# Kernel optimization log

Measured on AMD Instinct MI355X. Metric: run time of the kernel, lower is better.

## Reference

```python
import jax, jax.numpy as jnp
import numpy as np

N_NODES = 100000
N_EDGES = 1600000
D_IN = 256
HID = 128
OUT = 16
EPS = 1e-5


def _layer_norm(h, g, b):
    mu = jnp.mean(h, axis=-1, keepdims=True)
    var = jnp.mean((h - mu) ** 2, axis=-1, keepdims=True)
    return (h - mu) * jax.lax.rsqrt(var + EPS) * g + b


def _sage_conv(h, src, dst, Wn, bn, Wr):
    # mean-aggregate neighbor (source) features onto destination nodes
    msg = h[src]                                                # [E, F]
    s = jax.ops.segment_sum(msg, dst, num_segments=N_NODES)     # [N, F]
    cnt = jax.ops.segment_sum(jnp.ones((src.shape[0],), h.dtype), dst, num_segments=N_NODES)
    mean = s / jnp.maximum(cnt, 1.0)[:, None]
    return mean @ Wn + bn + h @ Wr                              # lin_l(agg) + lin_r(x)


def setup_inputs() -> dict:
    key = jax.random.key(0)
    ks = jax.random.split(key, 16)
    def lin(k, fi, fo):
        return jax.random.normal(k, (fi, fo), jnp.float32) / np.sqrt(fi)
    x = jax.random.normal(ks[0], (N_NODES, D_IN), jnp.float32)
    edge_index = jax.random.randint(ks[1], (2, N_EDGES), 0, N_NODES, dtype=jnp.int64)
    return {
        "x": x, "edge_index": edge_index,
        "W_nl0": lin(ks[2], D_IN, HID), "b_nl0": jnp.zeros((HID,), jnp.float32),
        "W_r0": lin(ks[3], D_IN, HID),
        "W_nl1": lin(ks[4], HID, HID), "b_nl1": jnp.zeros((HID,), jnp.float32),
        "W_r1": lin(ks[5], HID, HID),
        "g0": jnp.ones((HID,), jnp.float32), "be0": jnp.zeros((HID,), jnp.float32),
        "g1": jnp.ones((HID,), jnp.float32), "be1": jnp.zeros((HID,), jnp.float32),
        "W_jk": lin(ks[6], 2 * HID, HID), "b_jk": jnp.zeros((HID,), jnp.float32),
        "W_h1": lin(ks[7], HID, HID // 4), "b_h1": jnp.zeros((HID // 4,), jnp.float32),
        "W_h2": lin(ks[8], HID // 4, OUT), "b_h2": jnp.zeros((OUT,), jnp.float32),
    }


def reference(x, edge_index, W_nl0, b_nl0, W_r0, W_nl1, b_nl1, W_r1,
              g0, be0, g1, be1, W_jk, b_jk, W_h1, b_h1, W_h2, b_h2):
    src, dst = edge_index[0], edge_index[1]
    # layer 0: conv -> LayerNorm -> ReLU (dropout = identity in eval)
    h0 = jax.nn.relu(_layer_norm(_sage_conv(x, src, dst, W_nl0, b_nl0, W_r0), g0, be0))
    # layer 1
    h1 = jax.nn.relu(_layer_norm(_sage_conv(h0, src, dst, W_nl1, b_nl1, W_r1), g1, be1))
    # jumping-knowledge concat + projection to hidden_dim
    feats = jnp.concatenate([h0, h1], axis=-1) @ W_jk + b_jk
    # MLP head
    out = jax.nn.relu(feats @ W_h1 + b_h1) @ W_h2 + b_h2
    return out
```

## Files before the change

### kernel.cpp

```cpp
#include <hip/hip_runtime.h>
#include <hip/hip_bf16.h>

typedef __attribute__((ext_vector_type(8))) short bf16x8;
typedef __attribute__((ext_vector_type(4))) float f32x4;

static __device__ __forceinline__ float bf2f(__hip_bfloat16 v) { return __bfloat162float(v); }

static __device__ __forceinline__ float bs2f(short s) {
    unsigned u = ((unsigned)(unsigned short)s) << 16;
    float f; __builtin_memcpy(&f, &u, 4); return f;
}
static __device__ __forceinline__ short f2bs(float v) {
    __hip_bfloat16 b = __float2bfloat16(v);
    short s; __builtin_memcpy(&s, &b, 2); return s;
}
static __device__ __forceinline__ float loadf(const void* p, int i, bool f32) {
    if (f32) return ((const float*)p)[i];
    return bf2f(((const __hip_bfloat16*)p)[i]);
}

__global__ __launch_bounds__(256) void detect_kernel(const unsigned* __restrict__ ew,
        const unsigned short* __restrict__ xw, int* __restrict__ flags) {
    __shared__ int s_odd, s_f32;
    int t = threadIdx.x;
    if (t == 0) { s_odd = 0; s_f32 = 0; }
    __syncthreads();
    unsigned acc = 0;
    for (int i = t; i < 2048; i += 256) acc |= ew[2 * i + 1];
    if (acc) atomicOr(&s_odd, 1);
    int f32ev = 0;
    for (int i = t; i < 4096; i += 256) {
        unsigned e = (xw[i] >> 7) & 0xFF;
        if (e >= 0xC0) f32ev = 1;
    }
    if (f32ev) atomicOr(&s_f32, 1);
    __syncthreads();
    if (t == 0) { flags[0] = s_odd ? 0 : 1; flags[1] = s_f32; }
}


static __device__ __forceinline__ int dec_src(const unsigned* ew, int E, bool i64, int e) {
    return i64 ? (int)ew[2 * (size_t)e] : (int)ew[e];
}
static __device__ __forceinline__ int dec_dst(const unsigned* ew, int E, bool i64, int e) {
    return i64 ? (int)ew[2 * (size_t)E + 2 * (size_t)e] : (int)ew[(size_t)E + e];
}

__global__ __launch_bounds__(256) void coarse_count(const unsigned* __restrict__ ew, int E,
        const int* __restrict__ flags, int* __restrict__ ccnt) {
    __shared__ int h[512];
    int tid = threadIdx.x;
    for (int i = tid; i < 512; i += 256) h[i] = 0;
    __syncthreads();
    bool i64 = flags[0] != 0;
    int base = blockIdx.x * 8192;
    int lim = min(base + 8192, E);
    for (int e = base + tid; e < lim; e += 256)
        atomicAdd(&h[dec_dst(ew, E, i64, e) >> 8], 1);
    __syncthreads();
    for (int i = tid; i < 512; i += 256) if (h[i]) atomicAdd(&ccnt[i], h[i]);
}

__global__ __launch_bounds__(256) void coarse_scan(const int* __restrict__ ccnt,
        int* __restrict__ cbase, int* __restrict__ ccur, int NBINS) {
    __shared__ int part[256];
    int t = threadIdx.x;
    int v0 = (2 * t     < NBINS) ? ccnt[2 * t]     : 0;
    int v1 = (2 * t + 1 < NBINS) ? ccnt[2 * t + 1] : 0;
    int sum = v0 + v1;
    part[t] = sum;
    __syncthreads();
    for (int off = 1; off < 256; off <<= 1) {
        int u = (t >= off) ? part[t - off] : 0;
        __syncthreads();
        part[t] += u;
        __syncthreads();
    }
    int run = part[t] - sum;
    if (2 * t < NBINS)     { cbase[2 * t] = run;     ccur[2 * t] = run; }
    run += v0;
    if (2 * t + 1 < NBINS) { cbase[2 * t + 1] = run; ccur[2 * t + 1] = run; }
    if (t == 255) cbase[NBINS] = part[255];
}

__global__ __launch_bounds__(256) void coarse_scatter(const unsigned* __restrict__ ew, int E,
        const int* __restrict__ flags, int* __restrict__ ccur,
        uint2* __restrict__ pairs, int NBINS) {
    __shared__ int hist[512];
    __shared__ int hscan[513];
    __shared__ int fbase[512];
    __shared__ int part[256];
    __shared__ uint2 stage[2048];
    int tid = threadIdx.x;
    bool i64 = flags[0] != 0;
    int base = blockIdx.x * 2048;
    int cnt = min(2048, E - base);
    for (int i = tid; i < 512; i += 256) hist[i] = 0;
    __syncthreads();
    int myb[8], myo[8], mys[8], myd[8];
    #pragma unroll
    for (int j = 0; j < 8; ++j) {
        int e = base + j * 256 + tid;
        myb[j] = -1;
        if (e < E) {
            mys[j] = dec_src(ew, E, i64, e);
            int d = dec_dst(ew, E, i64, e);
            myd[j] = d & 255;
            myb[j] = d >> 8;
            myo[j] = atomicAdd(&hist[myb[j]], 1);
        }
    }
    __syncthreads();
    {
        int v0 = hist[2 * tid], v1 = hist[2 * tid + 1];
        int sum = v0 + v1;
        part[tid] = sum;
        __syncthreads();
        for (int off = 1; off < 256; off <<= 1) {
            int u = (tid >= off) ? part[tid - off] : 0;
            __syncthreads();
            part[tid] += u;
            __syncthreads();
        }
        int run = part[tid] - sum;
        hscan[2 * tid] = run;
        hscan[2 * tid + 1] = run + v0;
        if (tid == 255) hscan[512] = part[255];
    }
    __syncthreads();
    #pragma unroll
    for (int j = 0; j < 8; ++j)
        if (myb[j] >= 0) {
            uint2 p; p.x = (unsigned)mys[j]; p.y = (unsigned)myd[j];
            stage[hscan[myb[j]] + myo[j]] = p;
        }
    for (int i = tid; i < NBINS; i += 256) {
        int c = hist[i];
        if (c) fbase[i] = atomicAdd(&ccur[i], c);
    }
    __syncthreads();
    for (int i = tid; i < cnt; i += 256) {
        int lo = 0, hi = NBINS;
        while (hi - lo > 1) {
            int mid = (lo + hi) >> 1;
            if (hscan[mid] <= i) lo = mid; else hi = mid;
        }
        pairs[(size_t)fbase[lo] + (i - hscan[lo])] = stage[i];
    }
}

__global__ __launch_bounds__(256) void bin_degree(const uint2* __restrict__ pairs,
        const int* __restrict__ cbase, int* __restrict__ deg, int N) {
    __shared__ int dl[256];
    int tid = threadIdx.x, b = blockIdx.x;
    dl[tid] = 0;
    __syncthreads();
    int s = cbase[b], e = cbase[b + 1];
    for (int i = s + tid; i < e; i += 256) atomicAdd(&dl[pairs[i].y], 1);
    __syncthreads();
    int node = (b << 8) + tid;
    if (node < N) deg[node] = dl[tid];
}

__global__ __launch_bounds__(256) void bin_scatter(const uint2* __restrict__ pairs,
        const int* __restrict__ cbase, const int* __restrict__ rowptr,
        int* __restrict__ ebuf, int N) {
    __shared__ int cur[256];
    int tid = threadIdx.x, b = blockIdx.x;
    int node = (b << 8) + tid;
    cur[tid] = (node < N) ? rowptr[node] : 0;
    __syncthreads();
    int s = cbase[b], e = cbase[b + 1];
    for (int i = s + tid; i < e; i += 256) {
        uint2 p = pairs[i];
        int pos = atomicAdd(&cur[p.y], 1);
        ebuf[pos] = (int)p.x;
    }
}

__global__ __launch_bounds__(256) void scan_phaseA(const int* __restrict__ deg,
        int* __restrict__ blocksum, int N) {
    __shared__ int red[256];
    int i0 = blockIdx.x * 512 + threadIdx.x * 2;
    int s = 0;
    if (i0 < N)     s += deg[i0];
    if (i0 + 1 < N) s += deg[i0 + 1];
    red[threadIdx.x] = s;
    __syncthreads();
    for (int off = 128; off; off >>= 1) {
        if (threadIdx.x < off) red[threadIdx.x] += red[threadIdx.x + off];
        __syncthreads();
    }
    if (threadIdx.x == 0) blocksum[blockIdx.x] = red[0];
}

__global__ __launch_bounds__(256) void scan_phaseB(int* __restrict__ blocksum, int NB,
        int* __restrict__ rowptr, int N) {
    __shared__ int part[256];
    int t = threadIdx.x;
    int v[4]; int sum = 0;
    #pragma unroll
    for (int j = 0; j < 4; ++j) {
        int i = 4 * t + j;
        v[j] = (i < NB) ? blocksum[i] : 0;
        sum += v[j];
    }
    part[t] = sum;
    __syncthreads();
    for (int off = 1; off < 256; off <<= 1) {
        int u = (t >= off) ? part[t - off] : 0;
        __syncthreads();
        part[t] += u;
        __syncthreads();
    }
    int run = part[t] - sum;
    #pragma unroll
    for (int j = 0; j < 4; ++j) {
        int i = 4 * t + j;
        if (i < NB) blocksum[i] = run;
        run += v[j];
    }
    if (t == 255) rowptr[N] = part[255];
}

__global__ __launch_bounds__(256) void scan_phaseC(const int* __restrict__ deg,
        const int* __restrict__ blockoff, int* __restrict__ rowptr, int N) {
    __shared__ int part[256];
    int t = threadIdx.x;
    int i0 = blockIdx.x * 512 + 2 * t;
    int d0 = (i0 < N)     ? deg[i0]     : 0;
    int d1 = (i0 + 1 < N) ? deg[i0 + 1] : 0;
    int sum = d0 + d1;
    part[t] = sum;
    __syncthreads();
    for (int off = 1; off < 256; off <<= 1) {
        int u = (t >= off) ? part[t - off] : 0;
        __syncthreads();
        part[t] += u;
        __syncthreads();
    }
    int run = blockoff[blockIdx.x] + part[t] - sum;
    if (i0 < N)     rowptr[i0] = run;
    run += d0;
    if (i0 + 1 < N) rowptr[i0 + 1] = run;
}

__global__ void transpose_kernel(const void* __restrict__ W,
        __hip_bfloat16* __restrict__ Wt, int rows, int cols, int ldt,
        const int* __restrict__ flags) {
    int idx = blockIdx.x * blockDim.x + threadIdx.x;
    if (idx < rows * cols) {
        int fi = idx / cols, fo = idx % cols;
        Wt[fo * ldt + fi] = __float2bfloat16(loadf(W, idx, flags[1] != 0));
    }
}

template<int KSTEPS>
__global__ __launch_bounds__(256) void gemm_v6(
        const void* __restrict__ X0, const void* __restrict__ X1, int K0, int xflag,
        const __hip_bfloat16* __restrict__ Wt, const void* __restrict__ bias,
        void* __restrict__ outp, int ldo, int out_f32, int M, int Ncols,
        const int* __restrict__ flags) {
    constexpr int K = KSTEPS * 32;
    constexpr int CH = K / 8;
    constexpr int SITERS = (64 * CH) / 256;
    __shared__ short Wf[4 * KSTEPS * 64 * 8];
    bool pf = flags[1] != 0;
    bool xf32 = (xflag != 0) && pf;
    int tid = threadIdx.x;
    int wave = tid >> 6, lane = tid & 63;
    int quad = lane >> 4, r = lane & 15;
    int nodeA = blockIdx.x * 128 + wave * 32 + r;
    int nodeB = nodeA + 16;
    int nA = min(nodeA, M - 1);
    int nB = min(nodeB, M - 1);

    bf16x8 xfA[KSTEPS], xfB[KSTEPS];
    if (xf32) {
        #pragma unroll
        for (int ks = 0; ks < KSTEPS; ++ks) {
            int k = ks * 32 + quad * 8;
            const float* pA = (k < K0)
                ? ((const float*)X0 + (size_t)nA * K0 + k)
                : ((const float*)X1 + (size_t)nA * (K - K0) + (k - K0));
            const float* pB = (k < K0)
                ? ((const float*)X0 + (size_t)nB * K0 + k)
                : ((const float*)X1 + (size_t)nB * (K - K0) + (k - K0));
            float4 a0 = *(const float4*)pA;
            float4 a1 = *(const float4*)(pA + 4);
            float4 b0 = *(const float4*)pB;
            float4 b1 = *(const float4*)(pB + 4);
            bf16x8 ta, tb;
            ta[0] = f2bs(a0.x); ta[1] = f2bs(a0.y); ta[2] = f2bs(a0.z); ta[3] = f2bs(a0.w);
            ta[4] = f2bs(a1.x); ta[5] = f2bs(a1.y); ta[6] = f2bs(a1.z); ta[7] = f2bs(a1.w);
            tb[0] = f2bs(b0.x); tb[1] = f2bs(b0.y); tb[2] = f2bs(b0.z); tb[3] = f2bs(b0.w);
            tb[4] = f2bs(b1.x); tb[5] = f2bs(b1.y); tb[6] = f2bs(b1.z); tb[7] = f2bs(b1.w);
            xfA[ks] = ta;
            xfB[ks] = tb;
        }
    } else {
        #pragma unroll
        for (int ks = 0; ks < KSTEPS; ++ks) {
            int k = ks * 32 + quad * 8;
            const __hip_bfloat16* pA = (k < K0)
                ? ((const __hip_bfloat16*)X0 + (size_t)nA * K0 + k)
                : ((const __hip_bfloat16*)X1 + (size_t)nA * (K - K0) + (k - K0));
            const __hip_bfloat16* pB = (k < K0)
                ? ((const __hip_bfloat16*)X0 + (size_t)nB * K0 + k)
                : ((const __hip_bfloat16*)X1 + (size_t)nB * (K - K0) + (k - K0));
            xfA[ks] = *(const bf16x8*)pA;
            xfB[ks] = *(const bf16x8*)pB;
        }
    }

    int nphases = Ncols >> 6;
    for (int p = 0; p < nphases; ++p) {
        if (p) __syncthreads();
        #pragma unroll
        for (int i = 0; i < SITERS; ++i) {
            int idx = i * 256 + tid;
            int row_l = idx / CH, c = idx % CH;
            uint4 v = *(const uint4*)((const short*)Wt + (size_t)(p * 64 + row_l) * K + c * 8);
            int ftl = row_l >> 4, rr = row_l & 15;
            int ks = c >> 2, q = c & 3;
            int chunk = ((q * 16 + rr) ^ ks);
            *(uint4*)(Wf + (size_t)(((ftl * KSTEPS + ks) * 64) + chunk) * 8) = v;
        }
        __syncthreads();
        #pragma unroll
        for (int ftl = 0; ftl < 4; ++ftl) {
            f32x4 accA = {0.f, 0.f, 0.f, 0.f};
            f32x4 accB = {0.f, 0.f, 0.f, 0.f};
            #pragma unroll
            for (int ks = 0; ks < KSTEPS; ++ks) {
                bf16x8 wf = *(const bf16x8*)(Wf + (size_t)((ftl * KSTEPS + ks) * 64 + (lane ^ ks)) * 8);
                accA = __builtin_amdgcn_mfma_f32_16x16x32_bf16(wf, xfA[ks], accA, 0, 0, 0);
                accB = __builtin_amdgcn_mfma_f32_16x16x32_bf16(wf, xfB[ks], accB, 0, 0, 0);
            }
            int fo = p * 64 + ftl * 16 + quad * 4;
            float b0 = 0.f, b1 = 0.f, b2 = 0.f, b3 = 0.f;
            if (bias) {
                b0 = loadf(bias, fo + 0, pf); b1 = loadf(bias, fo + 1, pf);
                b2 = loadf(bias, fo + 2, pf); b3 = loadf(bias, fo + 3, pf);
            }
            if (out_f32) {
                if (nodeA < M) {
                    float4 res;
                    res.x = accA[0] + b0; res.y = accA[1] + b1;
                    res.z = accA[2] + b2; res.w = accA[3] + b3;
                    *(float4*)((float*)outp + (size_t)nodeA * ldo + fo) = res;
                }
                if (nodeB < M) {
                    float4 res;
                    res.x = accB[0] + b0; res.y = accB[1] + b1;
                    res.z = accB[2] + b2; res.w = accB[3] + b3;
                    *(float4*)((float*)outp + (size_t)nodeB * ldo + fo) = res;
                }
            } else {
                if (nodeA < M) {
                    short4 res;
                    res.x = f2bs(accA[0] + b0); res.y = f2bs(accA[1] + b1);
                    res.z = f2bs(accA[2] + b2); res.w = f2bs(accA[3] + b3);
                    *(short4*)((short*)outp + (size_t)nodeA * ldo + fo) = res;
                }
                if (nodeB < M) {
                    short4 res;
                    res.x = f2bs(accB[0] + b0); res.y = f2bs(accB[1] + b1);
                    res.z = f2bs(accB[2] + b2); res.w = f2bs(accB[3] + b3);
                    *(short4*)((short*)outp + (size_t)nodeB * ldo + fo) = res;
                }
            }
        }
    }
}

__global__ __launch_bounds__(256) void agg_ln_relu(
        const __hip_bfloat16* __restrict__ yz, const int* __restrict__ rowptr,
        const int* __restrict__ ebuf,
        const void* __restrict__ bn, const void* __restrict__ g,
        const void* __restrict__ be, __hip_bfloat16* __restrict__ hout, int N,
        const int* __restrict__ flags) {
    int node = (blockIdx.x * blockDim.x + threadIdx.x) >> 6;
    if (node >= N) return;
    node = __builtin_amdgcn_readfirstlane(node);
    bool pf = flags[1] != 0;
    int lane = threadIdx.x & 63;
    int f = lane * 2;
    const short* yzs = (const short*)yz;
    int start = rowptr[node], end = rowptr[node + 1];
    float a0 = 0.f, a1 = 0.f;
    int i = start;
    for (; i + 8 <= end; i += 8) {
        int n0 = ebuf[i + 0], n1 = ebuf[i + 1], n2 = ebuf[i + 2], n3 = ebuf[i + 3];
        int n4 = ebuf[i + 4], n5 = ebuf[i + 5], n6 = ebuf[i + 6], n7 = ebuf[i + 7];
        short2 t0 = *(const short2*)(yzs + (size_t)n0 * 256 + f);
        short2 t1 = *(const short2*)(yzs + (size_t)n1 * 256 + f);
        short2 t2 = *(const short2*)(yzs + (size_t)n2 * 256 + f);
        short2 t3 = *(const short2*)(yzs + (size_t)n3 * 256 + f);
        short2 t4 = *(const short2*)(yzs + (size_t)n4 * 256 + f);
        short2 t5 = *(const short2*)(yzs + (size_t)n5 * 256 + f);
        short2 t6 = *(const short2*)(yzs + (size_t)n6 * 256 + f);
        short2 t7 = *(const short2*)(yzs + (size_t)n7 * 256 + f);
        a0 += bs2f(t0.x) + bs2f(t1.x) + bs2f(t2.x) + bs2f(t3.x)
            + bs2f(t4.x) + bs2f(t5.x) + bs2f(t6.x) + bs2f(t7.x);
        a1 += bs2f(t0.y) + bs2f(t1.y) + bs2f(t2.y) + bs2f(t3.y)
            + bs2f(t4.y) + bs2f(t5.y) + bs2f(t6.y) + bs2f(t7.y);
    }
    for (; i + 2 <= end; i += 2) {
        int n0 = ebuf[i + 0], n1 = ebuf[i + 1];
        short2 t0 = *(const short2*)(yzs + (size_t)n0 * 256 + f);
        short2 t1 = *(const short2*)(yzs + (size_t)n1 * 256 + f);
        a0 += bs2f(t0.x) + bs2f(t1.x);
        a1 += bs2f(t0.y) + bs2f(t1.y);
    }
    if (i < end) {
        int n0 = ebuf[i];
        short2 t0 = *(const short2*)(yzs + (size_t)n0 * 256 + f);
        a0 += bs2f(t0.x);
        a1 += bs2f(t0.y);
    }
    float inv = 1.f / fmaxf((float)(end - start), 1.f);
    short2 zt = *(const short2*)(yzs + (size_t)node * 256 + 128 + f);
    float v0 = a0 * inv + loadf(bn, f, pf)     + bs2f(zt.x);
    float v1 = a1 * inv + loadf(bn, f + 1, pf) + bs2f(zt.y);
    float s = v0 + v1;
    #pragma unroll
    for (int off = 32; off > 0; off >>= 1) s += __shfl_xor(s, off, 64);
    float mu = s * (1.f / 128.f);
    float d0 = v0 - mu, d1 = v1 - mu;
    float q = d0 * d0 + d1 * d1;
    #pragma unroll
    for (int off = 32; off > 0; off >>= 1) q += __shfl_xor(q, off, 64);
    float rstd = rsqrtf(q * (1.f / 128.f) + 1e-5f);
    float o0 = fmaxf(d0 * rstd * loadf(g, f, pf)     + loadf(be, f, pf),     0.f);
    float o1 = fmaxf(d1 * rstd * loadf(g, f + 1, pf) + loadf(be, f + 1, pf), 0.f);
    short* hp = (short*)hout + (size_t)node * 128 + f;
    hp[0] = f2bs(o0);
    hp[1] = f2bs(o1);
}

__global__ __launch_bounds__(256) void head_kernel(
        const float* __restrict__ feats, const void* __restrict__ Wh1,
        const void* __restrict__ bh1, const void* __restrict__ Wh2,
        const void* __restrict__ bh2, void* __restrict__ outp, int N,
        const int* __restrict__ flags) {
    __shared__ float sfe[8 * 128];
    __shared__ float shid[8 * 32];
    bool pf = flags[1] != 0;
    int nb = blockIdx.x * 8;
    int tid = threadIdx.x;
    {
        int i = tid * 4;
        int gnode = nb + (i >> 7);
        float4 v = make_float4(0.f, 0.f, 0.f, 0.f);
        if (gnode < N) v = *(const float4*)(feats + (size_t)gnode * 128 + (i & 127));
        *(float4*)(sfe + i) = v;
    }
    __syncthreads();
    {
        int nloc = tid >> 5, col = tid & 31;
        float acc = loadf(bh1, col, pf);
        const float* fr = sfe + nloc * 128;
        #pragma unroll 8
        for (int k = 0; k < 128; ++k) acc += fr[k] * loadf(Wh1, k * 32 + col, pf);
        shid[nloc * 32 + col] = fmaxf(acc, 0.f);
    }
    __syncthreads();
    if (tid < 128) {
        int nloc = tid >> 4, col = tid & 15;
        int gnode = nb + nloc;
        if (gnode < N) {
            float acc = loadf(bh2, col, pf);
            const float* hr = shid + nloc * 32;
            #pragma unroll
            for (int k = 0; k < 32; ++k) acc += hr[k] * loadf(Wh2, k * 16 + col, pf);
            if (pf) ((float*)outp)[(size_t)gnode * 16 + col] = acc;
            else    ((__hip_bfloat16*)outp)[(size_t)gnode * 16 + col] = __float2bfloat16(acc);
        }
    }
}

extern "C" void kernel_launch(void* const* d_in, const int* in_sizes, int n_in,
                              void* d_out, int out_size, void* d_ws, size_t ws_size,
                              hipStream_t stream) {
    const void* x    = d_in[0];
    const unsigned* ei = (const unsigned*)d_in[1];
    const void* Wnl0 = d_in[2];
    const void* bnl0 = d_in[3];
    const void* Wr0  = d_in[4];
    const void* Wnl1 = d_in[5];
    const void* bnl1 = d_in[6];
    const void* Wr1  = d_in[7];
    const void* g0   = d_in[8];
    const void* be0  = d_in[9];
    const void* g1   = d_in[10];
    const void* be1  = d_in[11];
    const void* Wjk  = d_in[12];
    const void* bjk  = d_in[13];
    const void* Wh1  = d_in[14];
    const void* bh1  = d_in[15];
    const void* Wh2  = d_in[16];
    const void* bh2  = d_in[17];

    const int N = in_sizes[0] / 256;
    const int E = in_sizes[1] / 2;
    const int NBINS = (N + 255) >> 8;

    char* ws = (char*)d_ws;
    size_t off = 0;
    auto alloc = [&](size_t bytes) -> void* {
        void* p = ws + off;
        off = (off + bytes + 255) & ~(size_t)255;
        return p;
    };
    int* flags  = (int*)alloc(256);
    int* rowptr = (int*)alloc((size_t)(N + 1) * 4);
    int* deg    = (int*)alloc((size_t)N * 4);
    int* ebuf   = (int*)alloc((size_t)E * 4);
    int* blocksum = (int*)alloc(1024 * 4);
    int* ccnt   = (int*)alloc(512 * 4);
    int* cbase  = (int*)alloc(513 * 4);
    int* ccur   = (int*)alloc(512 * 4);
    uint2* pairs = (uint2*)alloc((size_t)E * 8);
    __hip_bfloat16* Wt0  = (__hip_bfloat16*)alloc(256 * 256 * 2);
    __hip_bfloat16* Wt1  = (__hip_bfloat16*)alloc(256 * 128 * 2);
    __hip_bfloat16* Wtjk = (__hip_bfloat16*)alloc(128 * 256 * 2);
    __hip_bfloat16* yz = (__hip_bfloat16*)alloc((size_t)N * 256 * 2);
    __hip_bfloat16* h0 = (__hip_bfloat16*)alloc((size_t)N * 128 * 2);
    __hip_bfloat16* h1 = (__hip_bfloat16*)alloc((size_t)N * 128 * 2);
    float* feats = (float*)yz;

    detect_kernel<<<1, 256, 0, stream>>>(ei, (const unsigned short*)x, flags);

    (void)hipMemsetAsync(ccnt, 0, 512 * 4, stream);
    coarse_count<<<(E + 8191) / 8192, 256, 0, stream>>>(ei, E, flags, ccnt);
    coarse_scan<<<1, 256, 0, stream>>>(ccnt, cbase, ccur, NBINS);
    coarse_scatter<<<(E + 2047) / 2048, 256, 0, stream>>>(ei, E, flags, ccur, pairs, NBINS);
    bin_degree<<<NBINS, 256, 0, stream>>>(pairs, cbase, deg, N);
    int NB = (N + 511) / 512;
    scan_phaseA<<<NB, 256, 0, stream>>>(deg, blocksum, N);
    scan_phaseB<<<1, 256, 0, stream>>>(blocksum, NB, rowptr, N);
    scan_phaseC<<<NB, 256, 0, stream>>>(deg, blocksum, rowptr, N);
    bin_scatter<<<NBINS, 256, 0, stream>>>(pairs, cbase, rowptr, ebuf, N);

    transpose_kernel<<<(256 * 128 + 255) / 256, 256, 0, stream>>>(Wnl0, Wt0, 256, 128, 256, flags);
    transpose_kernel<<<(256 * 128 + 255) / 256, 256, 0, stream>>>(Wr0,  Wt0 + 128 * 256, 256, 128, 256, flags);
    transpose_kernel<<<(128 * 128 + 255) / 256, 256, 0, stream>>>(Wnl1, Wt1, 128, 128, 128, flags);
    transpose_kernel<<<(128 * 128 + 255) / 256, 256, 0, stream>>>(Wr1,  Wt1 + 128 * 128, 128, 128, 128, flags);
    transpose_kernel<<<(256 * 128 + 255) / 256, 256, 0, stream>>>(Wjk,  Wtjk, 256, 128, 256, flags);

    int gblocks = (N + 127) / 128;
    int ablocks = (int)(((size_t)N * 64 + 255) / 256);

    gemm_v6<8><<<gblocks, 256, 0, stream>>>(x, x, 256, 1, Wt0, nullptr, yz, 256, 0, N, 256, flags);
    agg_ln_relu<<<ablocks, 256, 0, stream>>>(yz, rowptr, ebuf, bnl0, g0, be0, h0, N, flags);

    gemm_v6<4><<<gblocks, 256, 0, stream>>>(h0, h0, 128, 0, Wt1, nullptr, yz, 256, 0, N, 256, flags);
    agg_ln_relu<<<ablocks, 256, 0, stream>>>(yz, rowptr, ebuf, bnl1, g1, be1, h1, N, flags);

    gemm_v6<8><<<gblocks, 256, 0, stream>>>(h0, h1, 128, 0, Wtjk, bjk, feats, 128, 1, N, 128, flags);

    head_kernel<<<(N + 7) / 8, 256, 0, stream>>>(feats, Wh1, bh1, Wh2, bh2, d_out, N, flags);
}
```

Baseline: 574.1 us.

## Run MLP head first layer on MFMA with transposed bf16 weights

Replaces the scalar head kernel, which did 8 nodes per block with per-thread scalar dot products, with a version that handles 128 nodes per block. It converts feats to bf16 fragments and uses 16x16x32 bf16 MFMA for the 128->32 layer, staging a transposed Wh1 in swizzled LDS. The second 32->16 layer stays scalar, with vectorized output stores. This adds a small transpose launch and rounds the first-layer inputs to bf16, which may change accuracy slightly.

```diff
diff --git a/kernel.cpp b/kernel.cpp
--- a/kernel.cpp
+++ b/kernel.cpp
@@ -37,7 +37,6 @@
     __syncthreads();
     if (t == 0) { flags[0] = s_odd ? 0 : 1; flags[1] = s_f32; }
 }
-
 
 static __device__ __forceinline__ int dec_src(const unsigned* ew, int E, bool i64, int e) {
     return i64 ? (int)ew[2 * (size_t)e] : (int)ew[e];
@@ -439,43 +438,105 @@
     hp[1] = f2bs(o1);
 }
 
-__global__ __launch_bounds__(256) void head_kernel(
-        const float* __restrict__ feats, const void* __restrict__ Wh1,
+__global__ __launch_bounds__(256) void head_v2(
+        const float* __restrict__ feats, const __hip_bfloat16* __restrict__ Wth1,
         const void* __restrict__ bh1, const void* __restrict__ Wh2,
         const void* __restrict__ bh2, void* __restrict__ outp, int N,
         const int* __restrict__ flags) {
-    __shared__ float sfe[8 * 128];
-    __shared__ float shid[8 * 32];
+    constexpr int KSTEPS = 4;
+    constexpr int CH = 16;
+    constexpr int HS = 34;
+    __shared__ short Wf[2 * KSTEPS * 64 * 8];
+    __shared__ float hid[128 * HS];
     bool pf = flags[1] != 0;
-    int nb = blockIdx.x * 8;
     int tid = threadIdx.x;
-    {
-        int i = tid * 4;
-        int gnode = nb + (i >> 7);
-        float4 v = make_float4(0.f, 0.f, 0.f, 0.f);
-        if (gnode < N) v = *(const float4*)(feats + (size_t)gnode * 128 + (i & 127));
-        *(float4*)(sfe + i) = v;
-    }
-    __syncthreads();
-    {
-        int nloc = tid >> 5, col = tid & 31;
-        float acc = loadf(bh1, col, pf);
-        const float* fr = sfe + nloc * 128;
-        #pragma unroll 8
-        for (int k = 0; k < 128; ++k) acc += fr[k] * loadf(Wh1, k * 32 + col, pf);
-        shid[nloc * 32 + col] = fmaxf(acc, 0.f);
-    }
-    __syncthreads();
-    if (tid < 128) {
-        int nloc = tid >> 4, col = tid & 15;
-        int gnode = nb + nloc;
-        if (gnode < N) {
-            float acc = loadf(bh2, col, pf);
-            const float* hr = shid + nloc * 32;
-            #pragma unroll
-            for (int k = 0; k < 32; ++k) acc += hr[k] * loadf(Wh2, k * 16 + col, pf);
-            if (pf) ((float*)outp)[(size_t)gnode * 16 + col] = acc;
-            else    ((__hip_bfloat16*)outp)[(size_t)gnode * 16 + col] = __float2bfloat16(acc);
+    int wave = tid >> 6, lane = tid & 63;
+    int quad = lane >> 4, r = lane & 15;
+    int nodeA = blockIdx.x * 128 + wave * 32 + r;
+    int nodeB = nodeA + 16;
+    int nA = min(nodeA, N - 1);
+    int nB = min(nodeB, N - 1);
+
+    bf16x8 xfA[KSTEPS], xfB[KSTEPS];
+    #pragma unroll
+    for (int ks = 0; ks < KSTEPS; ++ks) {
+        int k = ks * 32 + quad * 8;
+        const float* pA = feats + (size_t)nA * 128 + k;
+        const float* pB = feats + (size_t)nB * 128 + k;
+        float4 a0 = *(const float4*)pA;
+        float4 a1 = *(const float4*)(pA + 4);
+        float4 b0 = *(const float4*)pB;
+        float4 b1 = *(const float4*)(pB + 4);
+        bf16x8 ta, tb;
+        ta[0] = f2bs(a0.x); ta[1] = f2bs(a0.y); ta[2] = f2bs(a0.z); ta[3] = f2bs(a0.w);
+        ta[4] = f2bs(a1.x); ta[5] = f2bs(a1.y); ta[6] = f2bs(a1.z); ta[7] = f2bs(a1.w);
+        tb[0] = f2bs(b0.x); tb[1] = f2bs(b0.y); tb[2] = f2bs(b0.z); tb[3] = f2bs(b0.w);
+        tb[4] = f2bs(b1.x); tb[5] = f2bs(b1.y); tb[6] = f2bs(b1.z); tb[7] = f2bs(b1.w);
+        xfA[ks] = ta;
+        xfB[ks] = tb;
+    }
+
+    #pragma unroll
+    for (int i = 0; i < 2; ++i) {
+        int idx = i * 256 + tid;
+        int row_l = idx / CH, c = idx % CH;
+        uint4 v = *(const uint4*)((const short*)Wth1 + (size_t)row_l * 128 + c * 8);
+        int ftl = row_l >> 4, rr = row_l & 15;
+        int ks = c >> 2, q = c & 3;
+        int chunk = ((q * 16 + rr) ^ ks);
+        *(uint4*)(Wf + (size_t)(((ftl * KSTEPS + ks) * 64) + chunk) * 8) = v;
+    }
+    __syncthreads();
+
+    #pragma unroll
+    for (int ftl = 0; ftl < 2; ++ftl) {
+        f32x4 accA = {0.f, 0.f, 0.f, 0.f};
+        f32x4 accB = {0.f, 0.f, 0.f, 0.f};
+        #pragma unroll
+        for (int ks = 0; ks < KSTEPS; ++ks) {
+            bf16x8 wf = *(const bf16x8*)(Wf + (size_t)((ftl * KSTEPS + ks) * 64 + (lane ^ ks)) * 8);
+            accA = __builtin_amdgcn_mfma_f32_16x16x32_bf16(wf, xfA[ks], accA, 0, 0, 0);
+            accB = __builtin_amdgcn_mfma_f32_16x16x32_bf16(wf, xfB[ks], accB, 0, 0, 0);
+        }
+        int fo = ftl * 16 + quad * 4;
+        float b0 = loadf(bh1, fo + 0, pf), b1 = loadf(bh1, fo + 1, pf);
+        float b2 = loadf(bh1, fo + 2, pf), b3 = loadf(bh1, fo + 3, pf);
+        float* hA = hid + (size_t)(wave * 32 + r) * HS + fo;
+        hA[0] = fmaxf(accA[0] + b0, 0.f); hA[1] = fmaxf(accA[1] + b1, 0.f);
+        hA[2] = fmaxf(accA[2] + b2, 0.f); hA[3] = fmaxf(accA[3] + b3, 0.f);
+        float* hB = hid + (size_t)(wave * 32 + 16 + r) * HS + fo;
+        hB[0] = fmaxf(accB[0] + b0, 0.f); hB[1] = fmaxf(accB[1] + b1, 0.f);
+        hB[2] = fmaxf(accB[2] + b2, 0.f); hB[3] = fmaxf(accB[3] + b3, 0.f);
+    }
+    __syncthreads();
+
+    int li = lane & 31, cg = lane >> 5;
+    int node = blockIdx.x * 128 + wave * 32 + li;
+    const float* hrow = hid + (size_t)(wave * 32 + li) * HS;
+    float acc[8];
+    #pragma unroll
+    for (int i = 0; i < 8; ++i) acc[i] = loadf(bh2, cg * 8 + i, pf);
+    #pragma unroll 4
+    for (int k = 0; k < 32; ++k) {
+        float hv = hrow[k];
+        #pragma unroll
+        for (int i = 0; i < 8; ++i)
+            acc[i] += hv * loadf(Wh2, k * 16 + cg * 8 + i, pf);
+    }
+    if (node < N) {
+        if (pf) {
+            float* op = (float*)outp + (size_t)node * 16 + cg * 8;
+            float4 r0 = {acc[0], acc[1], acc[2], acc[3]};
+            float4 r1 = {acc[4], acc[5], acc[6], acc[7]};
+            *(float4*)op = r0;
+            *(float4*)(op + 4) = r1;
+        } else {
+            short* op = (short*)outp + (size_t)node * 16 + cg * 8;
+            short4 r0, r1;
+            r0.x = f2bs(acc[0]); r0.y = f2bs(acc[1]); r0.z = f2bs(acc[2]); r0.w = f2bs(acc[3]);
+            r1.x = f2bs(acc[4]); r1.y = f2bs(acc[5]); r1.z = f2bs(acc[6]); r1.w = f2bs(acc[7]);
+            *(short4*)op = r0;
+            *(short4*)(op + 4) = r1;
         }
     }
 }
@@ -525,6 +586,7 @@
     __hip_bfloat16* Wt0  = (__hip_bfloat16*)alloc(256 * 256 * 2);
     __hip_bfloat16* Wt1  = (__hip_bfloat16*)alloc(256 * 128 * 2);
     __hip_bfloat16* Wtjk = (__hip_bfloat16*)alloc(128 * 256 * 2);
+    __hip_bfloat16* Wth1 = (__hip_bfloat16*)alloc(32 * 128 * 2);
     __hip_bfloat16* yz = (__hip_bfloat16*)alloc((size_t)N * 256 * 2);
     __hip_bfloat16* h0 = (__hip_bfloat16*)alloc((size_t)N * 128 * 2);
     __hip_bfloat16* h1 = (__hip_bfloat16*)alloc((size_t)N * 128 * 2);
@@ -548,6 +610,7 @@
     transpose_kernel<<<(128 * 128 + 255) / 256, 256, 0, stream>>>(Wnl1, Wt1, 128, 128, 128, flags);
     transpose_kernel<<<(128 * 128 + 255) / 256, 256, 0, stream>>>(Wr1,  Wt1 + 128 * 128, 128, 128, 128, flags);
     transpose_kernel<<<(256 * 128 + 255) / 256, 256, 0, stream>>>(Wjk,  Wtjk, 256, 128, 256, flags);
+    transpose_kernel<<<(128 * 32 + 255) / 256, 256, 0, stream>>>(Wh1,  Wth1, 128, 32, 128, flags);
 
     int gblocks = (N + 127) / 128;
     int ablocks = (int)(((size_t)N * 64 + 255) / 256);
@@ -560,5 +623,5 @@
 
     gemm_v6<8><<<gblocks, 256, 0, stream>>>(h0, h1, 128, 0, Wtjk, bjk, feats, 128, 1, N, 128, flags);
 
-    head_kernel<<<(N + 7) / 8, 256, 0, stream>>>(feats, Wh1, bh1, Wh2, bh2, d_out, N, flags);
-}
+    head_v2<<<gblocks, 256, 0, stream>>>(feats, Wth1, bh1, Wh2, bh2, d_out, N, flags);
+}
```

After: 530.6 us. -7.6%, faster.
